# Performance work log

Measured on AMD Instinct MI355X. Metric: run time of the kernel, lower is better.

## Reference

```python
import jax, jax.numpy as jnp
import numpy as np

B, N, D_IN, D_OUT = 16, 4096, 256, 128


def setup_inputs() -> dict:
    key = jax.random.key(0)
    ks = jax.random.split(key, 7)
    s_proj = float(np.sqrt(2.0 / D_IN))   # kaiming-ish scale
    s_mlp = float(np.sqrt(2.0 / D_OUT))
    return {
        "X": jax.random.normal(ks[0], (B, N, D_IN), dtype=jnp.float32),
        "W_proj": jax.random.normal(ks[1], (D_IN, D_OUT), dtype=jnp.float32) * s_proj,
        "b_proj": jnp.zeros((D_OUT,), dtype=jnp.float32),
        "W1": jax.random.normal(ks[2], (D_OUT, D_OUT), dtype=jnp.float32) * s_mlp,
        "b1": jnp.zeros((D_OUT,), dtype=jnp.float32),
        "W2": jax.random.normal(ks[3], (D_OUT, D_OUT), dtype=jnp.float32) * s_mlp,
        "b2": jnp.zeros((D_OUT,), dtype=jnp.float32),
    }


def reference(X, W_proj, b_proj, W1, b1, W2, b2):
    # proj: Linear(input_dim, output_dim)
    X = jnp.einsum("bnd,de->bne", X, W_proj) + b_proj
    # mlp: FeedForwardNetwork(D,D,D, num_layers=2) == Linear -> ReLU -> Linear
    X = jax.nn.relu(jnp.einsum("bnd,de->bne", X, W1) + b1)
    X = jnp.einsum("bnd,de->bne", X, W2) + b2
    # leave-one-out sum over the N axis: for each row i, sum of all rows j != i.
    # Identical math to the masked (B,N,N,D) expand-reduce in the torch source.
    return X.sum(axis=1, keepdims=True) - X
```

## Files before the change

### kernel.cpp

```cpp
#include <hip/hip_runtime.h>
#include <stdint.h>

#define D_IN  256
#define D_OUT 128
#define NSEQ  4096
#define NB    16
#define NBLK  1024
#define LDS_BYTES 32768

typedef __bf16 bf16x8 __attribute__((ext_vector_type(8)));
typedef float  f32x4  __attribute__((ext_vector_type(4)));

__device__ __forceinline__ unsigned short f2bf(float f) {
  __bf16 h = (__bf16)f;
  union { __bf16 h; unsigned short u; } c; c.h = h;
  return c.u;
}
__device__ __forceinline__ float bf2f(unsigned short u) {
  union { unsigned int u; float f; } a; a.u = ((unsigned int)u) << 16;
  return a.f;
}

__global__ __launch_bounds__(256) void prep(
    const float* __restrict__ Wp, const float* __restrict__ W1, const float* __restrict__ W2,
    const float* __restrict__ bp, const float* __restrict__ b1,
    unsigned short* __restrict__ WaT, unsigned short* __restrict__ W2T, float* __restrict__ be1) {
  int b = blockIdx.x;
  if (b < 128) {
    __shared__ float wp[256];
    int k0 = b * 2;
    wp[threadIdx.x] = Wp[k0 * 128 + threadIdx.x];
    __syncthreads();
    int kk = threadIdx.x >> 7, n = threadIdx.x & 127;
    float s = 0.f;
#pragma unroll 16
    for (int j = 0; j < 128; ++j) s += wp[kk * 128 + j] * W1[j * 128 + n];
    WaT[n * 256 + (k0 + kk)] = f2bf(s);
  } else if (b < 192) {
    int t = (b - 128) * 256 + threadIdx.x;
    int k = t >> 7, n = t & 127;
    W2T[n * 128 + k] = f2bf(W2[t]);
  } else {
    if (threadIdx.x < 128) {
      int n = threadIdx.x;
      float s = b1[n];
#pragma unroll 16
      for (int j = 0; j < 128; ++j) s += bp[j] * W1[j * 128 + n];
      be1[n] = s;
    }
  }
}

template <bool USE_WS>
__global__ __launch_bounds__(256, 4) void fused2(
    const float* __restrict__ X,
    const unsigned short* __restrict__ WaT,
    const unsigned short* __restrict__ W2T,
    const float* __restrict__ be1, const float* __restrict__ b2v,
    unsigned short* __restrict__ Y3, float* __restrict__ out, float* __restrict__ P) {
  extern __shared__ unsigned short smem[];
  unsigned short* bufA = smem;
  unsigned short* bufB = smem + 8192;

  const int tid  = threadIdx.x;
  const int lane = tid & 63;
  const int w    = tid >> 6;
  const int q    = lane >> 4;
  const int l16  = lane & 15;
  const int blk  = blockIdx.x;
  const int col0 = w * 32 + l16;
  const int col1 = col0 + 16;
  const int rowbase = blk * 64;

  const float e0  = be1[col0], e1  = be1[col1];
  const float bb0 = b2v[col0], bb1 = b2v[col1];

  f32x4 acc[4][2];
  bf16x8 bA[4][2], bB[4][2];

#pragma unroll
  for (int ks = 0; ks < 4; ++ks) {
    bA[ks][0] = *(const bf16x8*)(WaT + (size_t)col0 * 256 + ks * 32 + q * 8);
    bA[ks][1] = *(const bf16x8*)(WaT + (size_t)col1 * 256 + ks * 32 + q * 8);
  }

#pragma unroll
  for (int it = 0; it < 8; ++it) {
    int i = tid + it * 256;
    int r = i >> 5, c4 = (i & 31) << 2;
    const float4 v = *(const float4*)(X + (size_t)(rowbase + r) * D_IN + c4);
    ushort4 u; u.x = f2bf(v.x); u.y = f2bf(v.y); u.z = f2bf(v.z); u.w = f2bf(v.w);
    *(ushort4*)(bufA + r * 128 + ((((c4 >> 3) ^ (r & 15)) << 3) + (c4 & 7))) = u;
  }

  float4 xv[8];
#pragma unroll
  for (int it = 0; it < 8; ++it) {
    int i = tid + it * 256;
    int r = i >> 5, c4 = (i & 31) << 2;
    xv[it] = *(const float4*)(X + (size_t)(rowbase + r) * D_IN + 128 + c4);
  }

#pragma unroll
  for (int rt = 0; rt < 4; ++rt) {
    acc[rt][0] = (f32x4){0.f, 0.f, 0.f, 0.f};
    acc[rt][1] = (f32x4){0.f, 0.f, 0.f, 0.f};
  }
  __syncthreads();

#pragma unroll
  for (int ks = 0; ks < 4; ++ks) {
    bB[ks][0] = *(const bf16x8*)(WaT + (size_t)col0 * 256 + 128 + ks * 32 + q * 8);
    bB[ks][1] = *(const bf16x8*)(WaT + (size_t)col1 * 256 + 128 + ks * 32 + q * 8);
  }

#pragma unroll
  for (int ks = 0; ks < 4; ++ks)
#pragma unroll
    for (int rt = 0; rt < 4; ++rt) {
      bf16x8 a = *(const bf16x8*)(bufA + (rt * 16 + l16) * 128 + (((4 * ks + q) ^ l16) << 3));
      acc[rt][0] = __builtin_amdgcn_mfma_f32_16x16x32_bf16(a, bA[ks][0], acc[rt][0], 0, 0, 0);
      acc[rt][1] = __builtin_amdgcn_mfma_f32_16x16x32_bf16(a, bA[ks][1], acc[rt][1], 0, 0, 0);
    }

#pragma unroll
  for (int it = 0; it < 8; ++it) {
    int i = tid + it * 256;
    int r = i >> 5, c4 = (i & 31) << 2;
    ushort4 u; u.x = f2bf(xv[it].x); u.y = f2bf(xv[it].y); u.z = f2bf(xv[it].z); u.w = f2bf(xv[it].w);
    *(ushort4*)(bufB + r * 128 + ((((c4 >> 3) ^ (r & 15)) << 3) + (c4 & 7))) = u;
  }
  __syncthreads();

#pragma unroll
  for (int ks = 0; ks < 4; ++ks) {
    bA[ks][0] = *(const bf16x8*)(W2T + (size_t)col0 * 128 + ks * 32 + q * 8);
    bA[ks][1] = *(const bf16x8*)(W2T + (size_t)col1 * 128 + ks * 32 + q * 8);
  }

#pragma unroll
  for (int ks = 0; ks < 4; ++ks)
#pragma unroll
    for (int rt = 0; rt < 4; ++rt) {
      bf16x8 a = *(const bf16x8*)(bufB + (rt * 16 + l16) * 128 + (((4 * ks + q) ^ l16) << 3));
      acc[rt][0] = __builtin_amdgcn_mfma_f32_16x16x32_bf16(a, bB[ks][0], acc[rt][0], 0, 0, 0);
      acc[rt][1] = __builtin_amdgcn_mfma_f32_16x16x32_bf16(a, bB[ks][1], acc[rt][1], 0, 0, 0);
    }

#pragma unroll
  for (int rt = 0; rt < 4; ++rt)
#pragma unroll
    for (int r = 0; r < 4; ++r) {
      int row = rt * 16 + q * 4 + r;
      int sw = (row & 15) << 3;
      float v0 = acc[rt][0][r] + e0; v0 = v0 > 0.f ? v0 : 0.f;
      float v1 = acc[rt][1][r] + e1; v1 = v1 > 0.f ? v1 : 0.f;
      bufA[row * 128 + ((((col0 >> 3) << 3) ^ sw) + (col0 & 7))] = f2bf(v0);
      bufA[row * 128 + ((((col1 >> 3) << 3) ^ sw) + (col1 & 7))] = f2bf(v1);
    }
  __syncthreads();

#pragma unroll
  for (int rt = 0; rt < 4; ++rt) {
    acc[rt][0] = (f32x4){0.f, 0.f, 0.f, 0.f};
    acc[rt][1] = (f32x4){0.f, 0.f, 0.f, 0.f};
  }
#pragma unroll
  for (int ks = 0; ks < 4; ++ks)
#pragma unroll
    for (int rt = 0; rt < 4; ++rt) {
      bf16x8 a = *(const bf16x8*)(bufA + (rt * 16 + l16) * 128 + (((4 * ks + q) ^ l16) << 3));
      acc[rt][0] = __builtin_amdgcn_mfma_f32_16x16x32_bf16(a, bA[ks][0], acc[rt][0], 0, 0, 0);
      acc[rt][1] = __builtin_amdgcn_mfma_f32_16x16x32_bf16(a, bA[ks][1], acc[rt][1], 0, 0, 0);
    }

  float s0 = 0.f, s1 = 0.f;
#pragma unroll
  for (int rt = 0; rt < 4; ++rt)
#pragma unroll
    for (int r = 0; r < 4; ++r) {
      int row = rt * 16 + q * 4 + r;
      int sw = (row & 15) << 3;
      float v0 = acc[rt][0][r] + bb0;
      float v1 = acc[rt][1][r] + bb1;
      s0 += v0; s1 += v1;
      bufB[row * 128 + ((((col0 >> 3) << 3) ^ sw) + (col0 & 7))] = f2bf(v0);
      bufB[row * 128 + ((((col1 >> 3) << 3) ^ sw) + (col1 & 7))] = f2bf(v1);
    }
  __syncthreads();

  if (USE_WS) {
#pragma unroll
    for (int it = 0; it < 4; ++it) {
      int i = tid + it * 256;
      int r = i >> 4, g = i & 15;
      *(uint4*)(Y3 + (size_t)(rowbase + r) * 128 + g * 8) =
          *(const uint4*)(bufB + r * 128 + ((g ^ (r & 15)) << 3));
    }
  } else {
#pragma unroll
    for (int it = 0; it < 8; ++it) {
      int i = tid + it * 256;
      int r = i >> 5, c4 = (i & 31) << 2;
      ushort4 u = *(const ushort4*)(bufB + r * 128 + ((((c4 >> 3) ^ (r & 15)) << 3) + (c4 & 7)));
      float4 v; v.x = bf2f(u.x); v.y = bf2f(u.y); v.z = bf2f(u.z); v.w = bf2f(u.w);
      *(float4*)(out + (size_t)(rowbase + r) * D_OUT + c4) = v;
    }
  }

  s0 += __shfl_down(s0, 16); s0 += __shfl_down(s0, 32);
  s1 += __shfl_down(s1, 16); s1 += __shfl_down(s1, 32);
  if (lane < 16) {
    P[(size_t)blk * 128 + col0] = s0;
    P[(size_t)blk * 128 + col1] = s1;
  }
}

__global__ __launch_bounds__(256) void finalize_ws(
    float* __restrict__ out, const unsigned short* __restrict__ Y3, const float* __restrict__ P) {
  __shared__ float fs[256];
  const int tid  = threadIdx.x;
  const int row0 = blockIdx.x * 64;
  const int b    = row0 >> 12;
  {
    const int col = tid & 127;
    const int h   = tid >> 7;
    float s = 0.f;
    const float* p = P + (size_t)b * 64 * 128 + (size_t)h * 32 * 128 + col;
#pragma unroll
    for (int i = 0; i < 32; ++i) s += p[i * 128];
    fs[tid] = s;
  }
  __syncthreads();
  if (tid < 128) fs[tid] += fs[tid + 128];
  __syncthreads();

#pragma unroll
  for (int it = 0; it < 4; ++it) {
    int i = tid + it * 256;
    int r = i >> 4, g = (i & 15) * 8;
    size_t base = (size_t)(row0 + r) * 128 + g;
    uint4 u = *(const uint4*)(Y3 + base);
    float4 s0 = *(const float4*)(fs + g);
    float4 s1 = *(const float4*)(fs + g + 4);
    union { unsigned int uu; float f; } t;
    float4 o0, o1;
    t.uu = u.x << 16;          o0.x = s0.x - t.f;
    t.uu = u.x & 0xFFFF0000u;  o0.y = s0.y - t.f;
    t.uu = u.y << 16;          o0.z = s0.z - t.f;
    t.uu = u.y & 0xFFFF0000u;  o0.w = s0.w - t.f;
    t.uu = u.z << 16;          o1.x = s1.x - t.f;
    t.uu = u.z & 0xFFFF0000u;  o1.y = s1.y - t.f;
    t.uu = u.w << 16;          o1.z = s1.z - t.f;
    t.uu = u.w & 0xFFFF0000u;  o1.w = s1.w - t.f;
    *(float4*)(out + base) = o0;
    *(float4*)(out + base + 4) = o1;
  }
}

__global__ __launch_bounds__(256) void finalize_ip(
    float* __restrict__ out, const float* __restrict__ P) {
  __shared__ float fs[256];
  const int tid  = threadIdx.x;
  const int row0 = blockIdx.x * 64;
  const int b    = row0 >> 12;
  {
    const int col = tid & 127;
    const int h   = tid >> 7;
    float s = 0.f;
    const float* p = P + (size_t)b * 64 * 128 + (size_t)h * 32 * 128 + col;
#pragma unroll
    for (int i = 0; i < 32; ++i) s += p[i * 128];
    fs[tid] = s;
  }
  __syncthreads();
  if (tid < 128) fs[tid] += fs[tid + 128];
  __syncthreads();

#pragma unroll
  for (int it = 0; it < 4; ++it) {
    int i = tid + it * 256;
    int r = i >> 4, g = (i & 15) * 8;
    size_t base = (size_t)(row0 + r) * 128 + g;
    float4 s0 = *(const float4*)(fs + g);
    float4 s1 = *(const float4*)(fs + g + 4);
    float4 y0 = *(const float4*)(out + base);
    float4 y1 = *(const float4*)(out + base + 4);
    float4 o0, o1;
    o0.x = s0.x - y0.x; o0.y = s0.y - y0.y; o0.z = s0.z - y0.z; o0.w = s0.w - y0.w;
    o1.x = s1.x - y1.x; o1.y = s1.y - y1.y; o1.z = s1.z - y1.z; o1.w = s1.w - y1.w;
    *(float4*)(out + base) = o0;
    *(float4*)(out + base + 4) = o1;
  }
}

extern "C" void kernel_launch(void* const* d_in, const int* in_sizes, int n_in,
                              void* d_out, int out_size, void* d_ws, size_t ws_size,
                              hipStream_t stream) {
  const float* X  = (const float*)d_in[0];
  const float* Wp = (const float*)d_in[1];
  const float* bp = (const float*)d_in[2];
  const float* W1 = (const float*)d_in[3];
  const float* b1 = (const float*)d_in[4];
  const float* W2 = (const float*)d_in[5];
  const float* b2 = (const float*)d_in[6];
  float* out = (float*)d_out;

  char* ws = (char*)d_ws;
  float* be1          = (float*)ws;
  unsigned short* WaT = (unsigned short*)(ws + 4096);
  unsigned short* W2T = (unsigned short*)(ws + 4096 + 65536);
  float* P            = (float*)(ws + 4096 + 65536 + 32768);
  unsigned short* Y3  = (unsigned short*)(ws + 4096 + 65536 + 32768 + 524288);

  const size_t need = 4096 + 65536 + 32768 + 524288 + (size_t)NB * NSEQ * D_OUT * 2;
  const bool use_ws = ws_size >= need;

  prep<<<193, 256, 0, stream>>>(Wp, W1, W2, bp, b1, WaT, W2T, be1);

  if (use_ws) {
    fused2<true><<<NBLK, 256, LDS_BYTES, stream>>>(X, WaT, W2T, be1, b2, Y3, out, P);
    finalize_ws<<<NBLK, 256, 0, stream>>>(out, Y3, P);
  } else {
    fused2<false><<<NBLK, 256, LDS_BYTES, stream>>>(X, WaT, W2T, be1, b2, Y3, out, P);
    finalize_ip<<<NBLK, 256, 0, stream>>>(out, P);
  }
}
```

Measured before the change: 133.9 us.

## Give each wave its own rows, load X directly into registers, atomically reduce column sums

The fused kernel now assigns each wave 16 rows across all 128 output columns. The A operand is built straight from global X in registers, so the X staging through LDS and two of the barriers go away. B fragments are now reloaded from global or L2 per k-step instead of being held in registers. Per-block column sums are reduced in LDS and atomically added into a per-batch accumulator that prep zeroes, so the finalize kernels read 128 values instead of reducing 64 partials. The risks are more repeated weight loads, atomic contention (64 blocks per address) and non-deterministic summation order.

After: 163.9 us. +22.4%, slower.

```diff
diff --git a/kernel.cpp b/kernel.cpp
--- a/kernel.cpp
+++ b/kernel.cpp
@@ -6,7 +6,7 @@
 #define NSEQ  4096
 #define NB    16
 #define NBLK  1024
-#define LDS_BYTES 32768
+#define LDS_BYTES 34816
 
 typedef __bf16 bf16x8 __attribute__((ext_vector_type(8)));
 typedef float  f32x4  __attribute__((ext_vector_type(4)));
@@ -24,7 +24,8 @@
 __global__ __launch_bounds__(256) void prep(
     const float* __restrict__ Wp, const float* __restrict__ W1, const float* __restrict__ W2,
     const float* __restrict__ bp, const float* __restrict__ b1,
-    unsigned short* __restrict__ WaT, unsigned short* __restrict__ W2T, float* __restrict__ be1) {
+    unsigned short* __restrict__ WaT, unsigned short* __restrict__ W2T,
+    float* __restrict__ be1, float* __restrict__ S) {
   int b = blockIdx.x;
   if (b < 128) {
     __shared__ float wp[256];
@@ -47,6 +48,10 @@
 #pragma unroll 16
       for (int j = 0; j < 128; ++j) s += bp[j] * W1[j * 128 + n];
       be1[n] = s;
+    } else {
+      int i = threadIdx.x - 128;
+#pragma unroll
+      for (int j = 0; j < 16; ++j) S[i * 16 + j] = 0.f;
     }
   }
 }
@@ -57,10 +62,11 @@
     const unsigned short* __restrict__ WaT,
     const unsigned short* __restrict__ W2T,
     const float* __restrict__ be1, const float* __restrict__ b2v,
-    unsigned short* __restrict__ Y3, float* __restrict__ out, float* __restrict__ P) {
+    unsigned short* __restrict__ Y3, float* __restrict__ out, float* __restrict__ S) {
   extern __shared__ unsigned short smem[];
   unsigned short* bufA = smem;
   unsigned short* bufB = smem + 8192;
+  float* wsum = (float*)(smem + 16384);
 
   const int tid  = threadIdx.x;
   const int lane = tid & 63;
@@ -68,126 +74,82 @@
   const int q    = lane >> 4;
   const int l16  = lane & 15;
   const int blk  = blockIdx.x;
-  const int col0 = w * 32 + l16;
-  const int col1 = col0 + 16;
   const int rowbase = blk * 64;
-
-  const float e0  = be1[col0], e1  = be1[col1];
-  const float bb0 = b2v[col0], bb1 = b2v[col1];
-
-  f32x4 acc[4][2];
-  bf16x8 bA[4][2], bB[4][2];
+  const int myrow   = w * 16 + l16;
+
+  float e[8], bb[8];
+#pragma unroll
+  for (int ct = 0; ct < 8; ++ct) {
+    e[ct]  = be1[ct * 16 + l16];
+    bb[ct] = b2v[ct * 16 + l16];
+  }
+
+  f32x4 acc[8];
+#pragma unroll
+  for (int ct = 0; ct < 8; ++ct) acc[ct] = (f32x4){0.f, 0.f, 0.f, 0.f};
+
+  const float* xrow = X + (size_t)(rowbase + myrow) * D_IN;
+
+#pragma unroll
+  for (int ks = 0; ks < 8; ++ks) {
+    float4 lo = *(const float4*)(xrow + ks * 32 + q * 8);
+    float4 hi = *(const float4*)(xrow + ks * 32 + q * 8 + 4);
+    bf16x8 a;
+    a[0] = (__bf16)lo.x; a[1] = (__bf16)lo.y; a[2] = (__bf16)lo.z; a[3] = (__bf16)lo.w;
+    a[4] = (__bf16)hi.x; a[5] = (__bf16)hi.y; a[6] = (__bf16)hi.z; a[7] = (__bf16)hi.w;
+#pragma unroll
+    for (int ct = 0; ct < 8; ++ct) {
+      bf16x8 b = *(const bf16x8*)(WaT + (size_t)(ct * 16 + l16) * 256 + ks * 32 + q * 8);
+      acc[ct] = __builtin_amdgcn_mfma_f32_16x16x32_bf16(a, b, acc[ct], 0, 0, 0);
+    }
+  }
+
+#pragma unroll
+  for (int ct = 0; ct < 8; ++ct) {
+    int col = ct * 16 + l16;
+    int cb = (col >> 3) << 3, c7 = col & 7;
+#pragma unroll
+    for (int r = 0; r < 4; ++r) {
+      int row = w * 16 + q * 4 + r;
+      float v = acc[ct][r] + e[ct]; v = v > 0.f ? v : 0.f;
+      bufA[row * 128 + ((cb ^ ((row & 15) << 3)) + c7)] = f2bf(v);
+    }
+  }
+
+#pragma unroll
+  for (int ct = 0; ct < 8; ++ct) acc[ct] = (f32x4){0.f, 0.f, 0.f, 0.f};
 
 #pragma unroll
   for (int ks = 0; ks < 4; ++ks) {
-    bA[ks][0] = *(const bf16x8*)(WaT + (size_t)col0 * 256 + ks * 32 + q * 8);
-    bA[ks][1] = *(const bf16x8*)(WaT + (size_t)col1 * 256 + ks * 32 + q * 8);
-  }
-
-#pragma unroll
-  for (int it = 0; it < 8; ++it) {
-    int i = tid + it * 256;
-    int r = i >> 5, c4 = (i & 31) << 2;
-    const float4 v = *(const float4*)(X + (size_t)(rowbase + r) * D_IN + c4);
-    ushort4 u; u.x = f2bf(v.x); u.y = f2bf(v.y); u.z = f2bf(v.z); u.w = f2bf(v.w);
-    *(ushort4*)(bufA + r * 128 + ((((c4 >> 3) ^ (r & 15)) << 3) + (c4 & 7))) = u;
-  }
-
-  float4 xv[8];
-#pragma unroll
-  for (int it = 0; it < 8; ++it) {
-    int i = tid + it * 256;
-    int r = i >> 5, c4 = (i & 31) << 2;
-    xv[it] = *(const float4*)(X + (size_t)(rowbase + r) * D_IN + 128 + c4);
-  }
-
-#pragma unroll
-  for (int rt = 0; rt < 4; ++rt) {
-    acc[rt][0] = (f32x4){0.f, 0.f, 0.f, 0.f};
-    acc[rt][1] = (f32x4){0.f, 0.f, 0.f, 0.f};
+    bf16x8 a = *(const bf16x8*)(bufA + myrow * 128 + (((4 * ks + q) ^ l16) << 3));
+#pragma unroll
+    for (int ct = 0; ct < 8; ++ct) {
+      bf16x8 b = *(const bf16x8*)(W2T + (size_t)(ct * 16 + l16) * 128 + ks * 32 + q * 8);
+      acc[ct] = __builtin_amdgcn_mfma_f32_16x16x32_bf16(a, b, acc[ct], 0, 0, 0);
+    }
+  }
+
+#pragma unroll
+  for (int ct = 0; ct < 8; ++ct) {
+    int col = ct * 16 + l16;
+    int cb = (col >> 3) << 3, c7 = col & 7;
+    float s = 0.f;
+#pragma unroll
+    for (int r = 0; r < 4; ++r) {
+      int row = w * 16 + q * 4 + r;
+      float v = acc[ct][r] + bb[ct];
+      s += v;
+      bufB[row * 128 + ((cb ^ ((row & 15) << 3)) + c7)] = f2bf(v);
+    }
+    s += __shfl_down(s, 16); s += __shfl_down(s, 32);
+    if (lane < 16) wsum[w * 128 + col] = s;
   }
   __syncthreads();
 
-#pragma unroll
-  for (int ks = 0; ks < 4; ++ks) {
-    bB[ks][0] = *(const bf16x8*)(WaT + (size_t)col0 * 256 + 128 + ks * 32 + q * 8);
-    bB[ks][1] = *(const bf16x8*)(WaT + (size_t)col1 * 256 + 128 + ks * 32 + q * 8);
-  }
-
-#pragma unroll
-  for (int ks = 0; ks < 4; ++ks)
-#pragma unroll
-    for (int rt = 0; rt < 4; ++rt) {
-      bf16x8 a = *(const bf16x8*)(bufA + (rt * 16 + l16) * 128 + (((4 * ks + q) ^ l16) << 3));
-      acc[rt][0] = __builtin_amdgcn_mfma_f32_16x16x32_bf16(a, bA[ks][0], acc[rt][0], 0, 0, 0);
-      acc[rt][1] = __builtin_amdgcn_mfma_f32_16x16x32_bf16(a, bA[ks][1], acc[rt][1], 0, 0, 0);
-    }
-
-#pragma unroll
-  for (int it = 0; it < 8; ++it) {
-    int i = tid + it * 256;
-    int r = i >> 5, c4 = (i & 31) << 2;
-    ushort4 u; u.x = f2bf(xv[it].x); u.y = f2bf(xv[it].y); u.z = f2bf(xv[it].z); u.w = f2bf(xv[it].w);
-    *(ushort4*)(bufB + r * 128 + ((((c4 >> 3) ^ (r & 15)) << 3) + (c4 & 7))) = u;
-  }
-  __syncthreads();
-
-#pragma unroll
-  for (int ks = 0; ks < 4; ++ks) {
-    bA[ks][0] = *(const bf16x8*)(W2T + (size_t)col0 * 128 + ks * 32 + q * 8);
-    bA[ks][1] = *(const bf16x8*)(W2T + (size_t)col1 * 128 + ks * 32 + q * 8);
-  }
-
-#pragma unroll
-  for (int ks = 0; ks < 4; ++ks)
-#pragma unroll
-    for (int rt = 0; rt < 4; ++rt) {
-      bf16x8 a = *(const bf16x8*)(bufB + (rt * 16 + l16) * 128 + (((4 * ks + q) ^ l16) << 3));
-      acc[rt][0] = __builtin_amdgcn_mfma_f32_16x16x32_bf16(a, bB[ks][0], acc[rt][0], 0, 0, 0);
-      acc[rt][1] = __builtin_amdgcn_mfma_f32_16x16x32_bf16(a, bB[ks][1], acc[rt][1], 0, 0, 0);
-    }
-
-#pragma unroll
-  for (int rt = 0; rt < 4; ++rt)
-#pragma unroll
-    for (int r = 0; r < 4; ++r) {
-      int row = rt * 16 + q * 4 + r;
-      int sw = (row & 15) << 3;
-      float v0 = acc[rt][0][r] + e0; v0 = v0 > 0.f ? v0 : 0.f;
-      float v1 = acc[rt][1][r] + e1; v1 = v1 > 0.f ? v1 : 0.f;
-      bufA[row * 128 + ((((col0 >> 3) << 3) ^ sw) + (col0 & 7))] = f2bf(v0);
-      bufA[row * 128 + ((((col1 >> 3) << 3) ^ sw) + (col1 & 7))] = f2bf(v1);
-    }
-  __syncthreads();
-
-#pragma unroll
-  for (int rt = 0; rt < 4; ++rt) {
-    acc[rt][0] = (f32x4){0.f, 0.f, 0.f, 0.f};
-    acc[rt][1] = (f32x4){0.f, 0.f, 0.f, 0.f};
-  }
-#pragma unroll
-  for (int ks = 0; ks < 4; ++ks)
-#pragma unroll
-    for (int rt = 0; rt < 4; ++rt) {
-      bf16x8 a = *(const bf16x8*)(bufA + (rt * 16 + l16) * 128 + (((4 * ks + q) ^ l16) << 3));
-      acc[rt][0] = __builtin_amdgcn_mfma_f32_16x16x32_bf16(a, bA[ks][0], acc[rt][0], 0, 0, 0);
-      acc[rt][1] = __builtin_amdgcn_mfma_f32_16x16x32_bf16(a, bA[ks][1], acc[rt][1], 0, 0, 0);
-    }
-
-  float s0 = 0.f, s1 = 0.f;
-#pragma unroll
-  for (int rt = 0; rt < 4; ++rt)
-#pragma unroll
-    for (int r = 0; r < 4; ++r) {
-      int row = rt * 16 + q * 4 + r;
-      int sw = (row & 15) << 3;
-      float v0 = acc[rt][0][r] + bb0;
-      float v1 = acc[rt][1][r] + bb1;
-      s0 += v0; s1 += v1;
-      bufB[row * 128 + ((((col0 >> 3) << 3) ^ sw) + (col0 & 7))] = f2bf(v0);
-      bufB[row * 128 + ((((col1 >> 3) << 3) ^ sw) + (col1 & 7))] = f2bf(v1);
-    }
-  __syncthreads();
+  if (tid < 128) {
+    float s = wsum[tid] + wsum[128 + tid] + wsum[256 + tid] + wsum[384 + tid];
+    atomicAdd(&S[(size_t)(blk >> 6) * 128 + tid], s);
+  }
 
   if (USE_WS) {
 #pragma unroll
@@ -207,32 +169,15 @@
       *(float4*)(out + (size_t)(rowbase + r) * D_OUT + c4) = v;
     }
   }
-
-  s0 += __shfl_down(s0, 16); s0 += __shfl_down(s0, 32);
-  s1 += __shfl_down(s1, 16); s1 += __shfl_down(s1, 32);
-  if (lane < 16) {
-    P[(size_t)blk * 128 + col0] = s0;
-    P[(size_t)blk * 128 + col1] = s1;
-  }
 }
 
 __global__ __launch_bounds__(256) void finalize_ws(
-    float* __restrict__ out, const unsigned short* __restrict__ Y3, const float* __restrict__ P) {
-  __shared__ float fs[256];
+    float* __restrict__ out, const unsigned short* __restrict__ Y3, const float* __restrict__ S) {
+  __shared__ float fs[128];
   const int tid  = threadIdx.x;
   const int row0 = blockIdx.x * 64;
   const int b    = row0 >> 12;
-  {
-    const int col = tid & 127;
-    const int h   = tid >> 7;
-    float s = 0.f;
-    const float* p = P + (size_t)b * 64 * 128 + (size_t)h * 32 * 128 + col;
-#pragma unroll
-    for (int i = 0; i < 32; ++i) s += p[i * 128];
-    fs[tid] = s;
-  }
-  __syncthreads();
-  if (tid < 128) fs[tid] += fs[tid + 128];
+  if (tid < 128) fs[tid] = S[(size_t)b * 128 + tid];
   __syncthreads();
 
 #pragma unroll
@@ -259,22 +204,12 @@
 }
 
 __global__ __launch_bounds__(256) void finalize_ip(
-    float* __restrict__ out, const float* __restrict__ P) {
-  __shared__ float fs[256];
+    float* __restrict__ out, const float* __restrict__ S) {
+  __shared__ float fs[128];
   const int tid  = threadIdx.x;
   const int row0 = blockIdx.x * 64;
   const int b    = row0 >> 12;
-  {
-    const int col = tid & 127;
-    const int h   = tid >> 7;
-    float s = 0.f;
-    const float* p = P + (size_t)b * 64 * 128 + (size_t)h * 32 * 128 + col;
-#pragma unroll
-    for (int i = 0; i < 32; ++i) s += p[i * 128];
-    fs[tid] = s;
-  }
-  __syncthreads();
-  if (tid < 128) fs[tid] += fs[tid + 128];
+  if (tid < 128) fs[tid] = S[(size_t)b * 128 + tid];
   __syncthreads();
 
 #pragma unroll
@@ -307,22 +242,22 @@
   float* out = (float*)d_out;
 
   char* ws = (char*)d_ws;
-  float* be1          = (float*)ws;
-  unsigned short* WaT = (unsigned short*)(ws + 4096);
-  unsigned short* W2T = (unsigned short*)(ws + 4096 + 65536);
-  float* P            = (float*)(ws + 4096 + 65536 + 32768);
-  unsigned short* Y3  = (unsigned short*)(ws + 4096 + 65536 + 32768 + 524288);
-
-  const size_t need = 4096 + 65536 + 32768 + 524288 + (size_t)NB * NSEQ * D_OUT * 2;
+  float* S            = (float*)ws;
+  float* be1          = (float*)(ws + 8192);
+  unsigned short* WaT = (unsigned short*)(ws + 12288);
+  unsigned short* W2T = (unsigned short*)(ws + 12288 + 65536);
+  unsigned short* Y3  = (unsigned short*)(ws + 12288 + 65536 + 32768);
+
+  const size_t need = 12288 + 65536 + 32768 + (size_t)NB * NSEQ * D_OUT * 2;
   const bool use_ws = ws_size >= need;
 
-  prep<<<193, 256, 0, stream>>>(Wp, W1, W2, bp, b1, WaT, W2T, be1);
+  prep<<<193, 256, 0, stream>>>(Wp, W1, W2, bp, b1, WaT, W2T, be1, S);
 
   if (use_ws) {
-    fused2<true><<<NBLK, 256, LDS_BYTES, stream>>>(X, WaT, W2T, be1, b2, Y3, out, P);
-    finalize_ws<<<NBLK, 256, 0, stream>>>(out, Y3, P);
+    fused2<true><<<NBLK, 256, LDS_BYTES, stream>>>(X, WaT, W2T, be1, b2, Y3, out, S);
+    finalize_ws<<<NBLK, 256, 0, stream>>>(out, Y3, S);
   } else {
-    fused2<false><<<NBLK, 256, LDS_BYTES, stream>>>(X, WaT, W2T, be1, b2, Y3, out, P);
-    finalize_ip<<<NBLK, 256, 0, stream>>>(out, P);
-  }
-}
+    fused2<false><<<NBLK, 256, LDS_BYTES, stream>>>(X, WaT, W2T, be1, b2, Y3, out, S);
+    finalize_ip<<<NBLK, 256, 0, stream>>>(out, S);
+  }
+}
```

## Accumulate per-batch column sums with atomics and load both X halves upfront

Applied to the files above, without the earlier changes.

Per-block partial column sums are now reduced across warps in LDS and added with float atomics into a per-batch sum buffer, which prep zeroes. This removes the 32-way partial-sum reduction that every finalize block used to repeat. The fused kernel also loads both halves of X into registers and stages them to LDS together, dropping one barrier-separated phase. In exchange it adds register pressure, 2 KB more LDS per block, atomic contention (64 blocks per batch), and a summation order that is no longer deterministic.

After: 133.5 us. Within noise of the previous version (-0.3%).

```diff
diff --git a/kernel.cpp b/kernel.cpp
--- a/kernel.cpp
+++ b/kernel.cpp
@@ -6,7 +6,7 @@
 #define NSEQ  4096
 #define NB    16
 #define NBLK  1024
-#define LDS_BYTES 32768
+#define LDS_BYTES 34816
 
 typedef __bf16 bf16x8 __attribute__((ext_vector_type(8)));
 typedef float  f32x4  __attribute__((ext_vector_type(4)));
@@ -24,7 +24,8 @@
 __global__ __launch_bounds__(256) void prep(
     const float* __restrict__ Wp, const float* __restrict__ W1, const float* __restrict__ W2,
     const float* __restrict__ bp, const float* __restrict__ b1,
-    unsigned short* __restrict__ WaT, unsigned short* __restrict__ W2T, float* __restrict__ be1) {
+    unsigned short* __restrict__ WaT, unsigned short* __restrict__ W2T,
+    float* __restrict__ be1, float* __restrict__ S) {
   int b = blockIdx.x;
   if (b < 128) {
     __shared__ float wp[256];
@@ -47,6 +48,10 @@
 #pragma unroll 16
       for (int j = 0; j < 128; ++j) s += bp[j] * W1[j * 128 + n];
       be1[n] = s;
+    } else {
+      int i = threadIdx.x - 128;
+#pragma unroll
+      for (int j = 0; j < 16; ++j) S[i * 16 + j] = 0.f;
     }
   }
 }
@@ -57,10 +62,11 @@
     const unsigned short* __restrict__ WaT,
     const unsigned short* __restrict__ W2T,
     const float* __restrict__ be1, const float* __restrict__ b2v,
-    unsigned short* __restrict__ Y3, float* __restrict__ out, float* __restrict__ P) {
+    unsigned short* __restrict__ Y3, float* __restrict__ out, float* __restrict__ S) {
   extern __shared__ unsigned short smem[];
-  unsigned short* bufA = smem;
-  unsigned short* bufB = smem + 8192;
+  unsigned short* st0 = smem;
+  unsigned short* st1 = smem + 8192;
+  float* wsum = (float*)(smem + 16384);
 
   const int tid  = threadIdx.x;
   const int lane = tid & 63;
@@ -68,39 +74,41 @@
   const int q    = lane >> 4;
   const int l16  = lane & 15;
   const int blk  = blockIdx.x;
+  const int batch = blk >> 6;
+  const int rowbase = blk * 64;
   const int col0 = w * 32 + l16;
   const int col1 = col0 + 16;
-  const int rowbase = blk * 64;
 
   const float e0  = be1[col0], e1  = be1[col1];
   const float bb0 = b2v[col0], bb1 = b2v[col1];
 
   f32x4 acc[4][2];
   bf16x8 bA[4][2], bB[4][2];
+
+  float4 xv0[8], xv1[8];
+#pragma unroll
+  for (int it = 0; it < 8; ++it) {
+    int i = tid + it * 256;
+    int r = i >> 5, c4 = (i & 31) << 2;
+    xv0[it] = *(const float4*)(X + (size_t)(rowbase + r) * D_IN + c4);
+    xv1[it] = *(const float4*)(X + (size_t)(rowbase + r) * D_IN + 128 + c4);
+  }
+#pragma unroll
+  for (int it = 0; it < 8; ++it) {
+    int i = tid + it * 256;
+    int r = i >> 5, c4 = (i & 31) << 2;
+    int off = r * 128 + ((((c4 >> 3) ^ (r & 15)) << 3) + (c4 & 7));
+    ushort4 u0; u0.x = f2bf(xv0[it].x); u0.y = f2bf(xv0[it].y); u0.z = f2bf(xv0[it].z); u0.w = f2bf(xv0[it].w);
+    *(ushort4*)(st0 + off) = u0;
+    ushort4 u1; u1.x = f2bf(xv1[it].x); u1.y = f2bf(xv1[it].y); u1.z = f2bf(xv1[it].z); u1.w = f2bf(xv1[it].w);
+    *(ushort4*)(st1 + off) = u1;
+  }
 
 #pragma unroll
   for (int ks = 0; ks < 4; ++ks) {
     bA[ks][0] = *(const bf16x8*)(WaT + (size_t)col0 * 256 + ks * 32 + q * 8);
     bA[ks][1] = *(const bf16x8*)(WaT + (size_t)col1 * 256 + ks * 32 + q * 8);
   }
-
-#pragma unroll
-  for (int it = 0; it < 8; ++it) {
-    int i = tid + it * 256;
-    int r = i >> 5, c4 = (i & 31) << 2;
-    const float4 v = *(const float4*)(X + (size_t)(rowbase + r) * D_IN + c4);
-    ushort4 u; u.x = f2bf(v.x); u.y = f2bf(v.y); u.z = f2bf(v.z); u.w = f2bf(v.w);
-    *(ushort4*)(bufA + r * 128 + ((((c4 >> 3) ^ (r & 15)) << 3) + (c4 & 7))) = u;
-  }
-
-  float4 xv[8];
-#pragma unroll
-  for (int it = 0; it < 8; ++it) {
-    int i = tid + it * 256;
-    int r = i >> 5, c4 = (i & 31) << 2;
-    xv[it] = *(const float4*)(X + (size_t)(rowbase + r) * D_IN + 128 + c4);
-  }
-
 #pragma unroll
   for (int rt = 0; rt < 4; ++rt) {
     acc[rt][0] = (f32x4){0.f, 0.f, 0.f, 0.f};
@@ -118,19 +126,10 @@
   for (int ks = 0; ks < 4; ++ks)
 #pragma unroll
     for (int rt = 0; rt < 4; ++rt) {
-      bf16x8 a = *(const bf16x8*)(bufA + (rt * 16 + l16) * 128 + (((4 * ks + q) ^ l16) << 3));
+      bf16x8 a = *(const bf16x8*)(st0 + (rt * 16 + l16) * 128 + (((4 * ks + q) ^ l16) << 3));
       acc[rt][0] = __builtin_amdgcn_mfma_f32_16x16x32_bf16(a, bA[ks][0], acc[rt][0], 0, 0, 0);
       acc[rt][1] = __builtin_amdgcn_mfma_f32_16x16x32_bf16(a, bA[ks][1], acc[rt][1], 0, 0, 0);
     }
-
-#pragma unroll
-  for (int it = 0; it < 8; ++it) {
-    int i = tid + it * 256;
-    int r = i >> 5, c4 = (i & 31) << 2;
-    ushort4 u; u.x = f2bf(xv[it].x); u.y = f2bf(xv[it].y); u.z = f2bf(xv[it].z); u.w = f2bf(xv[it].w);
-    *(ushort4*)(bufB + r * 128 + ((((c4 >> 3) ^ (r & 15)) << 3) + (c4 & 7))) = u;
-  }
-  __syncthreads();
 
 #pragma unroll
   for (int ks = 0; ks < 4; ++ks) {
@@ -142,10 +141,11 @@
   for (int ks = 0; ks < 4; ++ks)
 #pragma unroll
     for (int rt = 0; rt < 4; ++rt) {
-      bf16x8 a = *(const bf16x8*)(bufB + (rt * 16 + l16) * 128 + (((4 * ks + q) ^ l16) << 3));
+      bf16x8 a = *(const bf16x8*)(st1 + (rt * 16 + l16) * 128 + (((4 * ks + q) ^ l16) << 3));
       acc[rt][0] = __builtin_amdgcn_mfma_f32_16x16x32_bf16(a, bB[ks][0], acc[rt][0], 0, 0, 0);
       acc[rt][1] = __builtin_amdgcn_mfma_f32_16x16x32_bf16(a, bB[ks][1], acc[rt][1], 0, 0, 0);
     }
+  __syncthreads();
 
 #pragma unroll
   for (int rt = 0; rt < 4; ++rt)
@@ -155,8 +155,8 @@
       int sw = (row & 15) << 3;
       float v0 = acc[rt][0][r] + e0; v0 = v0 > 0.f ? v0 : 0.f;
       float v1 = acc[rt][1][r] + e1; v1 = v1 > 0.f ? v1 : 0.f;
-      bufA[row * 128 + ((((col0 >> 3) << 3) ^ sw) + (col0 & 7))] = f2bf(v0);
-      bufA[row * 128 + ((((col1 >> 3) << 3) ^ sw) + (col1 & 7))] = f2bf(v1);
+      st0[row * 128 + ((((col0 >> 3) << 3) ^ sw) + (col0 & 7))] = f2bf(v0);
+      st0[row * 128 + ((((col1 >> 3) << 3) ^ sw) + (col1 & 7))] = f2bf(v1);
     }
   __syncthreads();
 
@@ -169,25 +169,38 @@
   for (int ks = 0; ks < 4; ++ks)
 #pragma unroll
     for (int rt = 0; rt < 4; ++rt) {
-      bf16x8 a = *(const bf16x8*)(bufA + (rt * 16 + l16) * 128 + (((4 * ks + q) ^ l16) << 3));
+      bf16x8 a = *(const bf16x8*)(st0 + (rt * 16 + l16) * 128 + (((4 * ks + q) ^ l16) << 3));
       acc[rt][0] = __builtin_amdgcn_mfma_f32_16x16x32_bf16(a, bA[ks][0], acc[rt][0], 0, 0, 0);
       acc[rt][1] = __builtin_amdgcn_mfma_f32_16x16x32_bf16(a, bA[ks][1], acc[rt][1], 0, 0, 0);
     }
 
-  float s0 = 0.f, s1 = 0.f;
-#pragma unroll
-  for (int rt = 0; rt < 4; ++rt)
-#pragma unroll
-    for (int r = 0; r < 4; ++r) {
-      int row = rt * 16 + q * 4 + r;
-      int sw = (row & 15) << 3;
-      float v0 = acc[rt][0][r] + bb0;
-      float v1 = acc[rt][1][r] + bb1;
-      s0 += v0; s1 += v1;
-      bufB[row * 128 + ((((col0 >> 3) << 3) ^ sw) + (col0 & 7))] = f2bf(v0);
-      bufB[row * 128 + ((((col1 >> 3) << 3) ^ sw) + (col1 & 7))] = f2bf(v1);
-    }
-  __syncthreads();
+  {
+    float s0 = 0.f, s1 = 0.f;
+#pragma unroll
+    for (int rt = 0; rt < 4; ++rt)
+#pragma unroll
+      for (int r = 0; r < 4; ++r) {
+        int row = rt * 16 + q * 4 + r;
+        int sw = (row & 15) << 3;
+        float v0 = acc[rt][0][r] + bb0;
+        float v1 = acc[rt][1][r] + bb1;
+        s0 += v0; s1 += v1;
+        st1[row * 128 + ((((col0 >> 3) << 3) ^ sw) + (col0 & 7))] = f2bf(v0);
+        st1[row * 128 + ((((col1 >> 3) << 3) ^ sw) + (col1 & 7))] = f2bf(v1);
+      }
+    s0 += __shfl_down(s0, 16); s0 += __shfl_down(s0, 32);
+    s1 += __shfl_down(s1, 16); s1 += __shfl_down(s1, 32);
+    if (lane < 16) {
+      wsum[w * 128 + col0] = s0;
+      wsum[w * 128 + col1] = s1;
+    }
+  }
+  __syncthreads();
+
+  if (tid < 128) {
+    float s = wsum[tid] + wsum[128 + tid] + wsum[256 + tid] + wsum[384 + tid];
+    atomicAdd(&S[(size_t)batch * 128 + tid], s);
+  }
 
   if (USE_WS) {
 #pragma unroll
@@ -195,44 +208,27 @@
       int i = tid + it * 256;
       int r = i >> 4, g = i & 15;
       *(uint4*)(Y3 + (size_t)(rowbase + r) * 128 + g * 8) =
-          *(const uint4*)(bufB + r * 128 + ((g ^ (r & 15)) << 3));
+          *(const uint4*)(st1 + r * 128 + ((g ^ (r & 15)) << 3));
     }
   } else {
 #pragma unroll
     for (int it = 0; it < 8; ++it) {
       int i = tid + it * 256;
       int r = i >> 5, c4 = (i & 31) << 2;
-      ushort4 u = *(const ushort4*)(bufB + r * 128 + ((((c4 >> 3) ^ (r & 15)) << 3) + (c4 & 7)));
+      ushort4 u = *(const ushort4*)(st1 + r * 128 + ((((c4 >> 3) ^ (r & 15)) << 3) + (c4 & 7)));
       float4 v; v.x = bf2f(u.x); v.y = bf2f(u.y); v.z = bf2f(u.z); v.w = bf2f(u.w);
       *(float4*)(out + (size_t)(rowbase + r) * D_OUT + c4) = v;
     }
   }
-
-  s0 += __shfl_down(s0, 16); s0 += __shfl_down(s0, 32);
-  s1 += __shfl_down(s1, 16); s1 += __shfl_down(s1, 32);
-  if (lane < 16) {
-    P[(size_t)blk * 128 + col0] = s0;
-    P[(size_t)blk * 128 + col1] = s1;
-  }
 }
 
 __global__ __launch_bounds__(256) void finalize_ws(
-    float* __restrict__ out, const unsigned short* __restrict__ Y3, const float* __restrict__ P) {
-  __shared__ float fs[256];
+    float* __restrict__ out, const unsigned short* __restrict__ Y3, const float* __restrict__ S) {
+  __shared__ float fs[128];
   const int tid  = threadIdx.x;
   const int row0 = blockIdx.x * 64;
   const int b    = row0 >> 12;
-  {
-    const int col = tid & 127;
-    const int h   = tid >> 7;
-    float s = 0.f;
-    const float* p = P + (size_t)b * 64 * 128 + (size_t)h * 32 * 128 + col;
-#pragma unroll
-    for (int i = 0; i < 32; ++i) s += p[i * 128];
-    fs[tid] = s;
-  }
-  __syncthreads();
-  if (tid < 128) fs[tid] += fs[tid + 128];
+  if (tid < 128) fs[tid] = S[(size_t)b * 128 + tid];
   __syncthreads();
 
 #pragma unroll
@@ -259,22 +255,12 @@
 }
 
 __global__ __launch_bounds__(256) void finalize_ip(
-    float* __restrict__ out, const float* __restrict__ P) {
-  __shared__ float fs[256];
+    float* __restrict__ out, const float* __restrict__ S) {
+  __shared__ float fs[128];
   const int tid  = threadIdx.x;
   const int row0 = blockIdx.x * 64;
   const int b    = row0 >> 12;
-  {
-    const int col = tid & 127;
-    const int h   = tid >> 7;
-    float s = 0.f;
-    const float* p = P + (size_t)b * 64 * 128 + (size_t)h * 32 * 128 + col;
-#pragma unroll
-    for (int i = 0; i < 32; ++i) s += p[i * 128];
-    fs[tid] = s;
-  }
-  __syncthreads();
-  if (tid < 128) fs[tid] += fs[tid + 128];
+  if (tid < 128) fs[tid] = S[(size_t)b * 128 + tid];
   __syncthreads();
 
 #pragma unroll
@@ -307,22 +293,22 @@
   float* out = (float*)d_out;
 
   char* ws = (char*)d_ws;
-  float* be1          = (float*)ws;
-  unsigned short* WaT = (unsigned short*)(ws + 4096);
-  unsigned short* W2T = (unsigned short*)(ws + 4096 + 65536);
-  float* P            = (float*)(ws + 4096 + 65536 + 32768);
-  unsigned short* Y3  = (unsigned short*)(ws + 4096 + 65536 + 32768 + 524288);
-
-  const size_t need = 4096 + 65536 + 32768 + 524288 + (size_t)NB * NSEQ * D_OUT * 2;
+  float* S            = (float*)ws;
+  float* be1          = (float*)(ws + 8192);
+  unsigned short* WaT = (unsigned short*)(ws + 12288);
+  unsigned short* W2T = (unsigned short*)(ws + 12288 + 65536);
+  unsigned short* Y3  = (unsigned short*)(ws + 12288 + 65536 + 32768);
+
+  const size_t need = 12288 + 65536 + 32768 + (size_t)NB * NSEQ * D_OUT * 2;
   const bool use_ws = ws_size >= need;
 
-  prep<<<193, 256, 0, stream>>>(Wp, W1, W2, bp, b1, WaT, W2T, be1);
+  prep<<<193, 256, 0, stream>>>(Wp, W1, W2, bp, b1, WaT, W2T, be1, S);
 
   if (use_ws) {
-    fused2<true><<<NBLK, 256, LDS_BYTES, stream>>>(X, WaT, W2T, be1, b2, Y3, out, P);
-    finalize_ws<<<NBLK, 256, 0, stream>>>(out, Y3, P);
+    fused2<true><<<NBLK, 256, LDS_BYTES, stream>>>(X, WaT, W2T, be1, b2, Y3, out, S);
+    finalize_ws<<<NBLK, 256, 0, stream>>>(out, Y3, S);
   } else {
-    fused2<false><<<NBLK, 256, LDS_BYTES, stream>>>(X, WaT, W2T, be1, b2, Y3, out, P);
-    finalize_ip<<<NBLK, 256, 0, stream>>>(out, P);
-  }
-}
+    fused2<false><<<NBLK, 256, LDS_BYTES, stream>>>(X, WaT, W2T, be1, b2, Y3, out, S);
+    finalize_ip<<<NBLK, 256, 0, stream>>>(out, S);
+  }
+}
```
